# Kernel optimization log

Hardware: AMD Instinct MI355X
Metric: run time of the kernel (lower is better)

Reference implementation:

```python
import jax, jax.numpy as jnp
import numpy as np

O, T, DIN, H, DOUT = 50000, 500000, 128, 256, 128


def setup_inputs() -> dict:
    key = jax.random.key(0)
    ks = jax.random.split(key, 12)
    s = 0.05
    return {
        "obj_vecs": jax.random.normal(ks[0], (O, DIN), jnp.float32),
        "pred_vecs": jax.random.normal(ks[1], (T, DIN), jnp.float32),
        "edges": jax.random.randint(ks[2], (T, 2), 0, O, jnp.int64),
        "w1a": jax.random.normal(ks[3], (3 * DIN, H), jnp.float32) * s,
        "b1a": jax.random.normal(ks[4], (H,), jnp.float32) * s,
        "w1b": jax.random.normal(ks[5], (H, 2 * H + DOUT), jnp.float32) * s,
        "b1b": jax.random.normal(ks[6], (2 * H + DOUT,), jnp.float32) * s,
        "w2a": jax.random.normal(ks[7], (H, H), jnp.float32) * s,
        "b2a": jax.random.normal(ks[8], (H,), jnp.float32) * s,
        "w2b": jax.random.normal(ks[9], (H, DOUT), jnp.float32) * s,
        "b2b": jax.random.normal(ks[10], (DOUT,), jnp.float32) * s,
    }


def reference(obj_vecs, pred_vecs, edges, w1a, b1a, w1b, b1b, w2a, b2a, w2b, b2b):
    n_obj = obj_vecs.shape[0]
    h_dim = w2a.shape[0]
    d_out = w2b.shape[1]
    s_idx = edges[:, 0]
    o_idx = edges[:, 1]
    # gather subject/object node features, concat with predicate: [T, 3*Din]
    cur_t = jnp.concatenate([obj_vecs[s_idx], pred_vecs, obj_vecs[o_idx]], axis=1)
    # edge MLP (net1): Linear-ReLU-Linear-ReLU -> [T, 2H + Dout]
    new_t = jax.nn.relu(jax.nn.relu(cur_t @ w1a + b1a) @ w1b + b1b)
    new_s = new_t[:, :h_dim]
    new_p = new_t[:, h_dim:h_dim + d_out]
    new_o = new_t[:, h_dim + d_out:]
    # scatter-add pooling back to nodes, both endpoints
    idx = jnp.concatenate([s_idx, o_idx])
    vals = jnp.concatenate([new_s, new_o], axis=0)
    pooled = jax.ops.segment_sum(vals, idx, num_segments=n_obj)
    # avg pooling: divide by per-node incidence count (clamped to >= 1)
    counts = jax.ops.segment_sum(jnp.ones(idx.shape[0], obj_vecs.dtype), idx,
                                 num_segments=n_obj)
    pooled = pooled / jnp.clip(counts, 1.0)[:, None]
    # node MLP (net2)
    new_obj = jax.nn.relu(jax.nn.relu(pooled @ w2a + b2a) @ w2b + b2b)
    return new_obj, new_p
```

## Files before the change

kernel.cpp:

```cpp
#include <hip/hip_runtime.h>


using f32x4 = __attribute__((ext_vector_type(4))) float;
using s16x8 = __attribute__((ext_vector_type(8))) short;
typedef unsigned short u16x8 __attribute__((ext_vector_type(8)));

#define VMCNT4  asm volatile("s_waitcnt vmcnt(4)" ::: "memory")
#define VMCNT8  asm volatile("s_waitcnt vmcnt(8)" ::: "memory")
#define VMCNT16 asm volatile("s_waitcnt vmcnt(16)" ::: "memory")
#define VMCNT20 asm volatile("s_waitcnt vmcnt(20)" ::: "memory")
#define VMCNT36 asm volatile("s_waitcnt vmcnt(36)" ::: "memory")
#define LGKM0   asm volatile("s_waitcnt lgkmcnt(0)" ::: "memory")
#define BAR     __builtin_amdgcn_s_barrier()
#define SCHEDB  __builtin_amdgcn_sched_barrier(0)

static __device__ __forceinline__ unsigned short f2b(float f) {
    unsigned int u = __float_as_uint(f);
    unsigned int r = (u + 0x7fffu + ((u >> 16) & 1u)) >> 16;
    return (unsigned short)r;
}

static __device__ __forceinline__ float b2f(unsigned short b) {
    return __uint_as_float(((unsigned)b) << 16);
}

static __device__ __forceinline__ unsigned swz(unsigned row, unsigned byteoff) {
    return byteoff ^ ((row & 7u) << 4);
}

static __device__ __forceinline__ void gload_lds16(const unsigned short* g, unsigned short* l) {
    __builtin_amdgcn_global_load_lds(
        (const __attribute__((address_space(1))) unsigned int*)g,
        (__attribute__((address_space(3))) unsigned int*)l,
        16, 0, 0);
}

__global__ void prep_weights(const float* __restrict__ w1a, const float* __restrict__ w1b,
                             const float* __restrict__ w2a, const float* __restrict__ w2b,
                             unsigned short* __restrict__ w1aT, unsigned short* __restrict__ w1bT,
                             unsigned short* __restrict__ w2aT, unsigned short* __restrict__ w2bT) {
    int t = blockIdx.x * blockDim.x + threadIdx.x;
    if (t < 6 * 16384) {
        int kt = t >> 14;
        int rem = t & 16383; int c = rem >> 6, kk = rem & 63;
        unsigned byte = ((unsigned)(c * 128 + kk * 2)) ^ ((c & 7u) << 4);
        *(unsigned short*)((char*)w1aT + (size_t)kt * 32768 + byte) =
            f2b(w1a[(size_t)(kt * 64 + kk) * 256 + c]);
        return;
    }
    t -= 98304;
    if (t < 10 * 16384) {
        int tile = t >> 14; int nc = tile >> 1, kh = tile & 1;
        int rem = t & 16383; int c = rem >> 7, kk = rem & 127;
        unsigned byte = ((unsigned)(c * 256 + kk * 2)) ^ ((c & 7u) << 4);
        *(unsigned short*)((char*)w1bT + (size_t)tile * 32768 + byte) =
            f2b(w1b[(size_t)(kh * 128 + kk) * 640 + nc * 128 + c]);
        return;
    }
    t -= 163840;
    if (t < 65536) { int n = t >> 8, k = t & 255; w2aT[t] = f2b(w2a[k * 256 + n]); return; }
    t -= 65536;
    if (t < 32768) { int n = t >> 8, k = t & 255; w2bT[t] = f2b(w2b[k * 128 + n]); return; }
}

__global__ void count_kernel_i(const int* __restrict__ edges, int* __restrict__ cnt, int T) {
    int e = blockIdx.x * blockDim.x + threadIdx.x;
    if (e < T) {
        atomicAdd(&cnt[edges[2 * (long long)e]], 1);
        atomicAdd(&cnt[edges[2 * (long long)e + 1]], 1);
    }
}

__global__ void scan_kernel(const int* __restrict__ cnt, int* __restrict__ rowptr,
                            int* __restrict__ cursor, int O) {
    __shared__ int sc[1024];
    const int tid = threadIdx.x;
    const int per = (O + 1023) >> 10;
    const int base = tid * per;
    int s = 0;
    for (int i = 0; i < per; ++i) { int j = base + i; if (j < O) s += cnt[j]; }
    sc[tid] = s;
    __syncthreads();
    for (int d = 1; d < 1024; d <<= 1) {
        int v = (tid >= d) ? sc[tid - d] : 0;
        __syncthreads();
        sc[tid] += v;
        __syncthreads();
    }
    int off = sc[tid] - s;
    for (int i = 0; i < per; ++i) {
        int j = base + i;
        if (j < O) { rowptr[j] = off; cursor[j] = off; off += cnt[j]; }
    }
    if (tid == 0) rowptr[O] = sc[1023];
}

__global__ void slot_kernel(const int* __restrict__ edges, int* __restrict__ cursor,
                            int* __restrict__ slotS, int* __restrict__ slotO, int T) {
    int e = blockIdx.x * blockDim.x + threadIdx.x;
    if (e < T) {
        int s = edges[2 * (long long)e];
        int o = edges[2 * (long long)e + 1];
        slotS[e] = atomicAdd(&cursor[s], 1);
        slotO[e] = atomicAdd(&cursor[o], 1);
    }
}

__global__ __launch_bounds__(512, 2) void edge_mlp(
    const float* __restrict__ obj, const float* __restrict__ pred,
    const int* __restrict__ edges,
    const unsigned short* __restrict__ w1aT, const float* __restrict__ b1a,
    const unsigned short* __restrict__ w1bT, const float* __restrict__ b1b,
    const int* __restrict__ slotS, const int* __restrict__ slotO,
    unsigned short* __restrict__ edgeout, float* __restrict__ outP, int T) {
    const int m0 = blockIdx.x * 128;
    const int tid = threadIdx.x;
    const int lane = tid & 63, wid = tid >> 6;
    const int wm = wid >> 2, wn = wid & 3;
    const bool evenL = ((lane & 1) == 0);

    __shared__ unsigned short U[81920];
    char* const ldsb = (char*)U;
    char* const bbase = ldsb + 65536;

    bool okR[4][4];
    #pragma unroll
    for (int mi = 0; mi < 4; ++mi)
        #pragma unroll
        for (int rr = 0; rr < 4; ++rr)
            okR[mi][rr] = (m0 + wm * 64 + mi * 16 + ((lane >> 4) << 2) + rr) < T;

    int slotSr[4][2], slotOr[4][2];
    #pragma unroll
    for (int mi = 0; mi < 4; ++mi)
        #pragma unroll
        for (int k = 0; k < 2; ++k) {
            int rsel = evenL ? k : 2 + k;
            int e = m0 + wm * 64 + mi * 16 + ((lane >> 4) << 2) + rsel;
            if (e >= T) e = T - 1;
            slotSr[mi][k] = slotS[e];
            slotOr[mi][k] = slotO[e];
        }

    const int r = tid >> 2;
    const int q = tid & 3;
    int e_r = m0 + r; if (e_r >= T) e_r = T - 1;
    const int sIdx_r = edges[2 * (long long)e_r];
    const int oIdx_r = edges[2 * (long long)e_r + 1];

    float bias1[4], bias2[5][2];
    #pragma unroll
    for (int nj = 0; nj < 4; ++nj) bias1[nj] = b1a[wn * 64 + nj * 16 + (lane & 15)];
    #pragma unroll
    for (int nc = 0; nc < 5; ++nc)
        #pragma unroll
        for (int nj = 0; nj < 2; ++nj)
            bias2[nc][nj] = b1b[nc * 128 + wn * 32 + nj * 16 + (lane & 15)];

    auto aSrc = [&](int kt) -> const float4* {
        const float* s;
        if (kt < 2)      s = obj  + (long long)sIdx_r * 128 + kt * 64;
        else if (kt < 4) s = pred + (long long)e_r   * 128 + (kt - 2) * 64;
        else             s = obj  + (long long)oIdx_r * 128 + (kt - 4) * 64;
        return (const float4*)s;
    };

    auto tp = [&](int i) -> const unsigned short* {
        return (i < 6) ? (w1aT + (size_t)i * 16384) : (w1bT + (size_t)(i - 6) * 16384);
    };

    auto stage32 = [&](const unsigned short* gt, char* bb) {
        #pragma unroll
        for (int rr4 = 0; rr4 < 4; ++rr4) {
            unsigned off = wid * 4096u + rr4 * 1024u;
            gload_lds16((const unsigned short*)((const char*)gt + off + lane * 16u),
                        (unsigned short*)(bb + off));
        }
    };

    auto writeA = [&](const float4* ap, char* ab) {
        #pragma unroll
        for (int i = 0; i < 4; ++i) {
            float4 v = ap[i];
            ushort4 pk; pk.x = f2b(v.x); pk.y = f2b(v.y); pk.z = f2b(v.z); pk.w = f2b(v.w);
            unsigned byte = (r * 128u + q * 32u + i * 8u) ^ ((r & 7u) << 4);
            *(ushort4*)(ab + byte) = pk;
        }
    };

    f32x4 acc1[4][4];
    #pragma unroll
    for (int a = 0; a < 4; ++a)
        #pragma unroll
        for (int b = 0; b < 4; ++b) acc1[a][b] = f32x4{0.f, 0.f, 0.f, 0.f};

    auto mfma1 = [&](const char* ab, const char* bb) {
        #pragma unroll
        for (int ks = 0; ks < 2; ++ks) {
            const unsigned kk = ks * 32u + ((lane >> 4) << 3);
            s16x8 af[4];
            #pragma unroll
            for (int mi = 0; mi < 4; ++mi) {
                unsigned row = wm * 64u + mi * 16u + (lane & 15);
                af[mi] = *(const s16x8*)(ab + ((row * 128u + kk * 2u) ^ ((row & 7u) << 4)));
            }
            #pragma unroll
            for (int nj = 0; nj < 4; ++nj) {
                unsigned c = wn * 64u + nj * 16u + (lane & 15);
                s16x8 bf = *(const s16x8*)(bb + ((c * 128u + kk * 2u) ^ ((c & 7u) << 4)));
                #pragma unroll
                for (int mi = 0; mi < 4; ++mi)
                    acc1[mi][nj] = __builtin_amdgcn_mfma_f32_16x16x32_bf16(af[mi], bf, acc1[mi][nj], 0, 0, 0);
            }
        }
    };

    float4 ap[4];
    {
        const float4* s4 = aSrc(0);
        #pragma unroll
        for (int i = 0; i < 4; ++i) ap[i] = s4[q * 4 + i];
    }
    writeA(ap, ldsb);
    stage32(tp(0), bbase);
    stage32(tp(1), bbase + 32768);
    {
        const float4* s4 = aSrc(1);
        #pragma unroll
        for (int i = 0; i < 4; ++i) ap[i] = s4[q * 4 + i];
    }
    VMCNT8;
    LGKM0; BAR; SCHEDB;

    #pragma unroll
    for (int s = 0; s < 6; ++s) {
        stage32(tp(s + 2), bbase + ((s + 2) % 3) * 32768);
        __builtin_amdgcn_s_setprio(1);
        mfma1(ldsb + (s & 1) * 16384, bbase + (s % 3) * 32768);
        __builtin_amdgcn_s_setprio(0);
        VMCNT4;
        if (s < 5) {
            writeA(ap, ldsb + ((s + 1) & 1) * 16384);
            if (s < 4) {
                const float4* s4 = aSrc(s + 2);
                #pragma unroll
                for (int i = 0; i < 4; ++i) ap[i] = s4[q * 4 + i];
            }
        }
        LGKM0; BAR; SCHEDB;
    }

    #pragma unroll
    for (int nj = 0; nj < 4; ++nj) {
        unsigned col = wn * 64u + nj * 16u + (lane & 15);
        #pragma unroll
        for (int mi = 0; mi < 4; ++mi)
            #pragma unroll
            for (int rr = 0; rr < 4; ++rr) {
                unsigned row = wm * 64u + mi * 16u + ((lane >> 4) << 2) + rr;
                float v = acc1[mi][nj][rr] + bias1[nj];
                v = v > 0.f ? v : 0.f;
                *(unsigned short*)(ldsb + ((row * 512u + col * 2u) ^ ((row & 7u) << 4))) = f2b(v);
            }
    }
    LGKM0; BAR; SCHEDB;

    #pragma unroll
    for (int nc = 0; nc < 5; ++nc) {
        f32x4 acc2[4][2];
        #pragma unroll
        for (int a = 0; a < 4; ++a)
            #pragma unroll
            for (int b = 0; b < 2; ++b) acc2[a][b] = f32x4{0.f, 0.f, 0.f, 0.f};

        #pragma unroll
        for (int kh = 0; kh < 2; ++kh) {
            const int s = 6 + nc * 2 + kh;
            if (s + 2 <= 15) stage32(tp(s + 2), bbase + ((s + 2) % 3) * 32768);
            const char* bb = bbase + (s % 3) * 32768;
            __builtin_amdgcn_s_setprio(1);
            #pragma unroll
            for (int ks = 0; ks < 4; ++ks) {
                const unsigned kkB = ks * 32u + ((lane >> 4) << 3);
                const unsigned kkH = (kh * 128u) + kkB;
                s16x8 af[4];
                #pragma unroll
                for (int mi = 0; mi < 4; ++mi) {
                    unsigned row = wm * 64u + mi * 16u + (lane & 15);
                    af[mi] = *(const s16x8*)(ldsb + ((row * 512u + kkH * 2u) ^ ((row & 7u) << 4)));
                }
                #pragma unroll
                for (int nj = 0; nj < 2; ++nj) {
                    unsigned c = wn * 32u + nj * 16u + (lane & 15);
                    s16x8 bf = *(const s16x8*)(bb + ((c * 256u + kkB * 2u) ^ ((c & 7u) << 4)));
                    #pragma unroll
                    for (int mi = 0; mi < 4; ++mi)
                        acc2[mi][nj] = __builtin_amdgcn_mfma_f32_16x16x32_bf16(af[mi], bf, acc2[mi][nj], 0, 0, 0);
                }
            }
            __builtin_amdgcn_s_setprio(0);

            if (kh == 0) {
                if (s == 6)       { VMCNT4; }
                else if (s == 12) { VMCNT36; }
                else if (s == 14) { VMCNT16; }
                else              { VMCNT20; }
                LGKM0; BAR; SCHEDB;
            }
        }

        if (nc == 2) {
            #pragma unroll
            for (int nj = 0; nj < 2; ++nj) {
                int col = 2 * 128 + wn * 32 + nj * 16 + (lane & 15);
                #pragma unroll
                for (int mi = 0; mi < 4; ++mi)
                    #pragma unroll
                    for (int rr = 0; rr < 4; ++rr) {
                        int row = wm * 64 + mi * 16 + ((lane >> 4) << 2) + rr;
                        if (okR[mi][rr]) {
                            float v = acc2[mi][nj][rr] + bias2[2][nj];
                            v = v > 0.f ? v : 0.f;
                            outP[(long long)(m0 + row) * 128 + (col - 256)] = v;
                        }
                    }
            }
            VMCNT36;
            LGKM0; BAR; SCHEDB;
        } else {
            #pragma unroll
            for (int nj = 0; nj < 2; ++nj) {
                int col = nc * 128 + wn * 32 + nj * 16 + (lane & 15);
                int pc = (nc < 2) ? col : (col - 384);
                int pcb = (lane & 1) ? (pc - 1) : pc;
                #pragma unroll
                for (int mi = 0; mi < 4; ++mi) {
                    float vv[4];
                    #pragma unroll
                    for (int rr = 0; rr < 4; ++rr) {
                        float v = acc2[mi][nj][rr] + bias2[nc][nj];
                        vv[rr] = v > 0.f ? v : 0.f;
                    }
                    float nb0 = __shfl_xor(vv[0], 1);
                    float nb1 = __shfl_xor(vv[1], 1);
                    float nb2 = __shfl_xor(vv[2], 1);
                    float nb3 = __shfl_xor(vv[3], 1);
                    #pragma unroll
                    for (int k = 0; k < 2; ++k) {
                        float lo = evenL ? (k ? vv[1] : vv[0]) : (k ? nb3 : nb2);
                        float hi = evenL ? (k ? nb1 : nb0) : (k ? vv[3] : vv[2]);
                        int rsel = evenL ? k : 2 + k;
                        if (okR[mi][rsel]) {
                            int slot = (nc < 2) ? slotSr[mi][k] : slotOr[mi][k];
                            unsigned pk = ((unsigned)f2b(hi) << 16) | f2b(lo);
                            *(unsigned*)(edgeout + (size_t)slot * 256 + pcb) = pk;
                        }
                    }
                }
            }
            if (nc < 4) {
                VMCNT20;
                LGKM0; BAR; SCHEDB;
            }
        }
    }
}

__global__ __launch_bounds__(256, 4) void pool_gather(
    const unsigned short* __restrict__ edgeout, const int* __restrict__ rowptr,
    unsigned short* __restrict__ pooled, int O) {
    int w = blockIdx.x * 4 + (threadIdx.x >> 6);
    if (w >= O) return;
    const int lane = threadIdx.x & 63;
    const int beg = rowptr[w], end = rowptr[w + 1];
    float ax = 0.f, ay = 0.f, az = 0.f, aw = 0.f;
    float bx = 0.f, by = 0.f, bz = 0.f, bw = 0.f;
    const unsigned short* base = edgeout + (size_t)beg * 256 + lane * 4;
    int n = end - beg;
    int i = 0;
    for (; i + 3 < n; i += 4) {
        ushort4 v0 = *(const ushort4*)(base + (size_t)(i    ) * 256);
        ushort4 v1 = *(const ushort4*)(base + (size_t)(i + 1) * 256);
        ushort4 v2 = *(const ushort4*)(base + (size_t)(i + 2) * 256);
        ushort4 v3 = *(const ushort4*)(base + (size_t)(i + 3) * 256);
        ax += b2f(v0.x); ay += b2f(v0.y); az += b2f(v0.z); aw += b2f(v0.w);
        bx += b2f(v1.x); by += b2f(v1.y); bz += b2f(v1.z); bw += b2f(v1.w);
        ax += b2f(v2.x); ay += b2f(v2.y); az += b2f(v2.z); aw += b2f(v2.w);
        bx += b2f(v3.x); by += b2f(v3.y); bz += b2f(v3.z); bw += b2f(v3.w);
    }
    for (; i < n; ++i) {
        ushort4 v0 = *(const ushort4*)(base + (size_t)i * 256);
        ax += b2f(v0.x); ay += b2f(v0.y); az += b2f(v0.z); aw += b2f(v0.w);
    }
    float inv = 1.f / fmaxf((float)n, 1.f);
    ushort4 o4;
    o4.x = f2b((ax + bx) * inv); o4.y = f2b((ay + by) * inv);
    o4.z = f2b((az + bz) * inv); o4.w = f2b((aw + bw) * inv);
    *(ushort4*)(pooled + (size_t)w * 256 + lane * 4) = o4;
}

__global__ __launch_bounds__(256, 2) void obj_mlp(
    const unsigned short* __restrict__ pooled,
    const unsigned short* __restrict__ w2aT, const float* __restrict__ b2a,
    const unsigned short* __restrict__ w2bT, const float* __restrict__ b2b,
    float* __restrict__ outObj, int O) {
    const int m0 = blockIdx.x * 64;
    const int tid = threadIdx.x;
    const int lane = tid & 63, wid = tid >> 6;
    const int wm = wid >> 1, wn = wid & 1;

    __shared__ unsigned short Abuf[64 * 256];

    {
        const int r = tid >> 2, q = tid & 3;
        int objc = m0 + r; if (objc >= O) objc = O - 1;
        const u16x8* s8 = (const u16x8*)(pooled + (size_t)objc * 256);
        #pragma unroll
        for (int i = 0; i < 8; ++i) {
            u16x8 v = s8[q * 8 + i];
            unsigned byte = r * 512u + (q * 64u + i * 8u) * 2u;
            *(u16x8*)((char*)Abuf + swz(r, byte)) = v;
        }
    }
    __syncthreads();

    f32x4 acc1[2][2][4];
    #pragma unroll
    for (int a = 0; a < 2; ++a)
        #pragma unroll
        for (int b = 0; b < 2; ++b)
            #pragma unroll
            for (int c = 0; c < 4; ++c) acc1[a][b][c] = f32x4{0.f, 0.f, 0.f, 0.f};
    #pragma unroll
    for (int ks = 0; ks < 8; ++ks) {
        const int klane = ks * 32 + ((lane >> 4) << 3);
        s16x8 af[2];
        #pragma unroll
        for (int mi = 0; mi < 2; ++mi) {
            int row = wm * 32 + mi * 16 + (lane & 15);
            af[mi] = *(const s16x8*)((const char*)Abuf + swz(row, row * 512u + klane * 2u));
        }
        #pragma unroll
        for (int nb = 0; nb < 2; ++nb)
            #pragma unroll
            for (int nj = 0; nj < 4; ++nj) {
                int col = nb * 128 + wn * 64 + nj * 16 + (lane & 15);
                s16x8 bf = *(const s16x8*)(w2aT + (long long)col * 256 + klane);
                #pragma unroll
                for (int mi = 0; mi < 2; ++mi)
                    acc1[nb][mi][nj] = __builtin_amdgcn_mfma_f32_16x16x32_bf16(af[mi], bf, acc1[nb][mi][nj], 0, 0, 0);
            }
    }
    __syncthreads();

    #pragma unroll
    for (int nb = 0; nb < 2; ++nb)
        #pragma unroll
        for (int nj = 0; nj < 4; ++nj) {
            int col = nb * 128 + wn * 64 + nj * 16 + (lane & 15);
            float bias = b2a[col];
            #pragma unroll
            for (int mi = 0; mi < 2; ++mi)
                #pragma unroll
                for (int rr = 0; rr < 4; ++rr) {
                    int row = wm * 32 + mi * 16 + ((lane >> 4) << 2) + rr;
                    float v = acc1[nb][mi][nj][rr] + bias;
                    v = v > 0.f ? v : 0.f;
                    *(unsigned short*)((char*)Abuf + swz(row, row * 512u + col * 2u)) = f2b(v);
                }
        }
    __syncthreads();

    f32x4 acc2[2][4];
    #pragma unroll
    for (int b = 0; b < 2; ++b)
        #pragma unroll
        for (int c = 0; c < 4; ++c) acc2[b][c] = f32x4{0.f, 0.f, 0.f, 0.f};
    #pragma unroll
    for (int ks = 0; ks < 8; ++ks) {
        const int klane = ks * 32 + ((lane >> 4) << 3);
        s16x8 af[2];
        #pragma unroll
        for (int mi = 0; mi < 2; ++mi) {
            int row = wm * 32 + mi * 16 + (lane & 15);
            af[mi] = *(const s16x8*)((const char*)Abuf + swz(row, row * 512u + klane * 2u));
        }
        #pragma unroll
        for (int nj = 0; nj < 4; ++nj) {
            int col = wn * 64 + nj * 16 + (lane & 15);
            s16x8 bf = *(const s16x8*)(w2bT + (long long)col * 256 + klane);
            #pragma unroll
            for (int mi = 0; mi < 2; ++mi)
                acc2[mi][nj] = __builtin_amdgcn_mfma_f32_16x16x32_bf16(af[mi], bf, acc2[mi][nj], 0, 0, 0);
        }
    }

    #pragma unroll
    for (int nj = 0; nj < 4; ++nj) {
        int col = wn * 64 + nj * 16 + (lane & 15);
        float bias = b2b[col];
        #pragma unroll
        for (int mi = 0; mi < 2; ++mi)
            #pragma unroll
            for (int rr = 0; rr < 4; ++rr) {
                int row = wm * 32 + mi * 16 + ((lane >> 4) << 2) + rr;
                int o = m0 + row;
                if (o < O) {
                    float v = acc2[mi][nj][rr] + bias;
                    v = v > 0.f ? v : 0.f;
                    outObj[(long long)o * 128 + col] = v;
                }
            }
    }
}

extern "C" void kernel_launch(void* const* d_in, const int* in_sizes, int n_in,
                              void* d_out, int out_size, void* d_ws, size_t ws_size,
                              hipStream_t stream) {
    const float* obj  = (const float*)d_in[0];
    const float* pred = (const float*)d_in[1];
    const int*   edges = (const int*)d_in[2];
    const float* w1a = (const float*)d_in[3];
    const float* b1a = (const float*)d_in[4];
    const float* w1b = (const float*)d_in[5];
    const float* b1b = (const float*)d_in[6];
    const float* w2a = (const float*)d_in[7];
    const float* b2a = (const float*)d_in[8];
    const float* w2b = (const float*)d_in[9];
    const float* b2b = (const float*)d_in[10];

    const int O = in_sizes[0] / 128;
    const int T = in_sizes[1] / 128;

    auto al = [](size_t x) { return (x + 255) & ~(size_t)255; };
    const size_t szEdgeout = (size_t)2 * T * 256 * 2;
    const size_t szPooled  = (size_t)O * 256 * 2;
    const size_t szCnt     = (size_t)O * 4;
    const size_t szRow     = (size_t)(O + 1) * 4;
    const size_t szSlot    = (size_t)T * 4;

    size_t off = 0;
    char* ws = (char*)d_ws;
    unsigned short* edgeout = (unsigned short*)(ws + off); off += al(szEdgeout);
    unsigned short* pooled  = (unsigned short*)(ws + off); off += al(szPooled);
    int* cnt    = (int*)(ws + off); off += al(szCnt);
    int* cursor = (int*)(ws + off); off += al(szCnt);
    int* rowptr = (int*)(ws + off); off += al(szRow);
    int* slotS  = (int*)(ws + off); off += al(szSlot);
    int* slotO  = (int*)(ws + off); off += al(szSlot);
    unsigned short* w1aT = (unsigned short*)(ws + off); off += (size_t)6 * 16384 * 2;
    unsigned short* w1bT = (unsigned short*)(ws + off); off += (size_t)10 * 16384 * 2;
    unsigned short* w2aT = (unsigned short*)(ws + off); off += (size_t)256 * 256 * 2;
    unsigned short* w2bT = (unsigned short*)(ws + off);

    float* outObj = (float*)d_out;
    float* outP   = (float*)d_out + (size_t)O * 128;

    hipMemsetAsync(cnt, 0, szCnt, stream);
    const int prepElems = 98304 + 163840 + 65536 + 32768;
    prep_weights<<<(prepElems + 255) / 256, 256, 0, stream>>>(w1a, w1b, w2a, w2b, w1aT, w1bT, w2aT, w2bT);
    count_kernel_i<<<(T + 255) / 256, 256, 0, stream>>>(edges, cnt, T);
    scan_kernel<<<1, 1024, 0, stream>>>(cnt, rowptr, cursor, O);
    slot_kernel<<<(T + 255) / 256, 256, 0, stream>>>(edges, cursor, slotS, slotO, T);
    edge_mlp<<<(T + 127) / 128, 512, 0, stream>>>(obj, pred, edges, w1aT, b1a, w1bT, b1b, slotS, slotO, edgeout, outP, T);
    pool_gather<<<(O + 3) / 4, 256, 0, stream>>>(edgeout, rowptr, pooled, O);
    obj_mlp<<<(O + 63) / 64, 256, 0, stream>>>(pooled, w2aT, b2a, w2bT, b2b, outObj, O);
}
```

Before: 917.1 us.

## Fuse pooling gather into node MLP and merge count with slot assignment

The CSR slot assignment now takes the return value of the counting atomics as a local offset, and a cheap fixup pass adds rowptr afterwards. This removes the separate cursor array and one of the two atomic passes. Pool averaging is moved into obj_mlp, which gathers and averages each node's edge rows straight into swizzled LDS. That drops the pooled intermediate buffer and a kernel launch. The cost is that obj_mlp now does a latency-bound gather with fewer waves per row block (launch bounds 2 versus 4), which may hide memory latency less well.

```diff
diff --git a/kernel.cpp b/kernel.cpp
--- a/kernel.cpp
+++ b/kernel.cpp
@@ -63,16 +63,16 @@
     if (t < 32768) { int n = t >> 8, k = t & 255; w2bT[t] = f2b(w2b[k * 128 + n]); return; }
 }
 
-__global__ void count_kernel_i(const int* __restrict__ edges, int* __restrict__ cnt, int T) {
+__global__ void count_slot_kernel(const int* __restrict__ edges, int* __restrict__ cnt,
+                                  int* __restrict__ slotS, int* __restrict__ slotO, int T) {
     int e = blockIdx.x * blockDim.x + threadIdx.x;
     if (e < T) {
-        atomicAdd(&cnt[edges[2 * (long long)e]], 1);
-        atomicAdd(&cnt[edges[2 * (long long)e + 1]], 1);
-    }
-}
-
-__global__ void scan_kernel(const int* __restrict__ cnt, int* __restrict__ rowptr,
-                            int* __restrict__ cursor, int O) {
+        slotS[e] = atomicAdd(&cnt[edges[2 * (long long)e]], 1);
+        slotO[e] = atomicAdd(&cnt[edges[2 * (long long)e + 1]], 1);
+    }
+}
+
+__global__ void scan_kernel(const int* __restrict__ cnt, int* __restrict__ rowptr, int O) {
     __shared__ int sc[1024];
     const int tid = threadIdx.x;
     const int per = (O + 1023) >> 10;
@@ -90,19 +90,17 @@
     int off = sc[tid] - s;
     for (int i = 0; i < per; ++i) {
         int j = base + i;
-        if (j < O) { rowptr[j] = off; cursor[j] = off; off += cnt[j]; }
+        if (j < O) { rowptr[j] = off; off += cnt[j]; }
     }
     if (tid == 0) rowptr[O] = sc[1023];
 }
 
-__global__ void slot_kernel(const int* __restrict__ edges, int* __restrict__ cursor,
-                            int* __restrict__ slotS, int* __restrict__ slotO, int T) {
+__global__ void fixup_kernel(const int* __restrict__ edges, const int* __restrict__ rowptr,
+                             int* __restrict__ slotS, int* __restrict__ slotO, int T) {
     int e = blockIdx.x * blockDim.x + threadIdx.x;
     if (e < T) {
-        int s = edges[2 * (long long)e];
-        int o = edges[2 * (long long)e + 1];
-        slotS[e] = atomicAdd(&cursor[s], 1);
-        slotO[e] = atomicAdd(&cursor[o], 1);
+        slotS[e] += rowptr[edges[2 * (long long)e]];
+        slotO[e] += rowptr[edges[2 * (long long)e + 1]];
     }
 }
 
@@ -366,41 +364,8 @@
     }
 }
 
-__global__ __launch_bounds__(256, 4) void pool_gather(
+__global__ __launch_bounds__(256, 2) void obj_mlp(
     const unsigned short* __restrict__ edgeout, const int* __restrict__ rowptr,
-    unsigned short* __restrict__ pooled, int O) {
-    int w = blockIdx.x * 4 + (threadIdx.x >> 6);
-    if (w >= O) return;
-    const int lane = threadIdx.x & 63;
-    const int beg = rowptr[w], end = rowptr[w + 1];
-    float ax = 0.f, ay = 0.f, az = 0.f, aw = 0.f;
-    float bx = 0.f, by = 0.f, bz = 0.f, bw = 0.f;
-    const unsigned short* base = edgeout + (size_t)beg * 256 + lane * 4;
-    int n = end - beg;
-    int i = 0;
-    for (; i + 3 < n; i += 4) {
-        ushort4 v0 = *(const ushort4*)(base + (size_t)(i    ) * 256);
-        ushort4 v1 = *(const ushort4*)(base + (size_t)(i + 1) * 256);
-        ushort4 v2 = *(const ushort4*)(base + (size_t)(i + 2) * 256);
-        ushort4 v3 = *(const ushort4*)(base + (size_t)(i + 3) * 256);
-        ax += b2f(v0.x); ay += b2f(v0.y); az += b2f(v0.z); aw += b2f(v0.w);
-        bx += b2f(v1.x); by += b2f(v1.y); bz += b2f(v1.z); bw += b2f(v1.w);
-        ax += b2f(v2.x); ay += b2f(v2.y); az += b2f(v2.z); aw += b2f(v2.w);
-        bx += b2f(v3.x); by += b2f(v3.y); bz += b2f(v3.z); bw += b2f(v3.w);
-    }
-    for (; i < n; ++i) {
-        ushort4 v0 = *(const ushort4*)(base + (size_t)i * 256);
-        ax += b2f(v0.x); ay += b2f(v0.y); az += b2f(v0.z); aw += b2f(v0.w);
-    }
-    float inv = 1.f / fmaxf((float)n, 1.f);
-    ushort4 o4;
-    o4.x = f2b((ax + bx) * inv); o4.y = f2b((ay + by) * inv);
-    o4.z = f2b((az + bz) * inv); o4.w = f2b((aw + bw) * inv);
-    *(ushort4*)(pooled + (size_t)w * 256 + lane * 4) = o4;
-}
-
-__global__ __launch_bounds__(256, 2) void obj_mlp(
-    const unsigned short* __restrict__ pooled,
     const unsigned short* __restrict__ w2aT, const float* __restrict__ b2a,
     const unsigned short* __restrict__ w2bT, const float* __restrict__ b2b,
     float* __restrict__ outObj, int O) {
@@ -411,16 +376,38 @@
 
     __shared__ unsigned short Abuf[64 * 256];
 
-    {
-        const int r = tid >> 2, q = tid & 3;
-        int objc = m0 + r; if (objc >= O) objc = O - 1;
-        const u16x8* s8 = (const u16x8*)(pooled + (size_t)objc * 256);
-        #pragma unroll
-        for (int i = 0; i < 8; ++i) {
-            u16x8 v = s8[q * 8 + i];
-            unsigned byte = r * 512u + (q * 64u + i * 8u) * 2u;
-            *(u16x8*)((char*)Abuf + swz(r, byte)) = v;
-        }
+    for (int it = 0; it < 16; ++it) {
+        const int row = it * 4 + wid;
+        const int oI = m0 + row;
+        float ax = 0.f, ay = 0.f, az = 0.f, aw = 0.f;
+        float bx = 0.f, by = 0.f, bz = 0.f, bw = 0.f;
+        int n = 0;
+        if (oI < O) {
+            const int beg = rowptr[oI];
+            n = rowptr[oI + 1] - beg;
+            const unsigned short* base = edgeout + (size_t)beg * 256 + lane * 4;
+            int i = 0;
+            for (; i + 3 < n; i += 4) {
+                ushort4 v0 = *(const ushort4*)(base + (size_t)(i    ) * 256);
+                ushort4 v1 = *(const ushort4*)(base + (size_t)(i + 1) * 256);
+                ushort4 v2 = *(const ushort4*)(base + (size_t)(i + 2) * 256);
+                ushort4 v3 = *(const ushort4*)(base + (size_t)(i + 3) * 256);
+                ax += b2f(v0.x); ay += b2f(v0.y); az += b2f(v0.z); aw += b2f(v0.w);
+                bx += b2f(v1.x); by += b2f(v1.y); bz += b2f(v1.z); bw += b2f(v1.w);
+                ax += b2f(v2.x); ay += b2f(v2.y); az += b2f(v2.z); aw += b2f(v2.w);
+                bx += b2f(v3.x); by += b2f(v3.y); bz += b2f(v3.z); bw += b2f(v3.w);
+            }
+            for (; i < n; ++i) {
+                ushort4 v0 = *(const ushort4*)(base + (size_t)i * 256);
+                ax += b2f(v0.x); ay += b2f(v0.y); az += b2f(v0.z); aw += b2f(v0.w);
+            }
+        }
+        float inv = 1.f / fmaxf((float)n, 1.f);
+        ushort4 pk;
+        pk.x = f2b((ax + bx) * inv); pk.y = f2b((ay + by) * inv);
+        pk.z = f2b((az + bz) * inv); pk.w = f2b((aw + bw) * inv);
+        unsigned byte = ((unsigned)row * 512u + (unsigned)lane * 8u) ^ (((unsigned)row & 7u) << 4);
+        *(ushort4*)((char*)Abuf + byte) = pk;
     }
     __syncthreads();
 
@@ -534,7 +521,6 @@
 
     auto al = [](size_t x) { return (x + 255) & ~(size_t)255; };
     const size_t szEdgeout = (size_t)2 * T * 256 * 2;
-    const size_t szPooled  = (size_t)O * 256 * 2;
     const size_t szCnt     = (size_t)O * 4;
     const size_t szRow     = (size_t)(O + 1) * 4;
     const size_t szSlot    = (size_t)T * 4;
@@ -542,9 +528,7 @@
     size_t off = 0;
     char* ws = (char*)d_ws;
     unsigned short* edgeout = (unsigned short*)(ws + off); off += al(szEdgeout);
-    unsigned short* pooled  = (unsigned short*)(ws + off); off += al(szPooled);
     int* cnt    = (int*)(ws + off); off += al(szCnt);
-    int* cursor = (int*)(ws + off); off += al(szCnt);
     int* rowptr = (int*)(ws + off); off += al(szRow);
     int* slotS  = (int*)(ws + off); off += al(szSlot);
     int* slotO  = (int*)(ws + off); off += al(szSlot);
@@ -559,10 +543,9 @@
     hipMemsetAsync(cnt, 0, szCnt, stream);
     const int prepElems = 98304 + 163840 + 65536 + 32768;
     prep_weights<<<(prepElems + 255) / 256, 256, 0, stream>>>(w1a, w1b, w2a, w2b, w1aT, w1bT, w2aT, w2bT);
-    count_kernel_i<<<(T + 255) / 256, 256, 0, stream>>>(edges, cnt, T);
-    scan_kernel<<<1, 1024, 0, stream>>>(cnt, rowptr, cursor, O);
-    slot_kernel<<<(T + 255) / 256, 256, 0, stream>>>(edges, cursor, slotS, slotO, T);
+    count_slot_kernel<<<(T + 255) / 256, 256, 0, stream>>>(edges, cnt, slotS, slotO, T);
+    scan_kernel<<<1, 1024, 0, stream>>>(cnt, rowptr, O);
+    fixup_kernel<<<(T + 255) / 256, 256, 0, stream>>>(edges, rowptr, slotS, slotO, T);
     edge_mlp<<<(T + 127) / 128, 512, 0, stream>>>(obj, pred, edges, w1aT, b1a, w1bT, b1b, slotS, slotO, edgeout, outP, T);
-    pool_gather<<<(O + 3) / 4, 256, 0, stream>>>(edgeout, rowptr, pooled, O);
-    obj_mlp<<<(O + 63) / 64, 256, 0, stream>>>(pooled, w2aT, b2a, w2bT, b2b, outObj, O);
-}
+    obj_mlp<<<(O + 63) / 64, 256, 0, stream>>>(edgeout, rowptr, w2aT, b2a, w2bT, b2b, outObj, O);
+}
```

Result: no change. 901.8 us (-1.7%).
